# Kernel optimization log

Hardware: AMD Instinct MI355X
Metric: run time of the kernel (lower is better)

## Reference

```python
import jax, jax.numpy as jnp
import numpy as np

N_EMB = 1024
EMB_DIM = 256
BETA = 0.25


def setup_inputs() -> dict:
    key = jax.random.key(0)
    k1, k2 = jax.random.split(key)
    z = jax.random.normal(k1, (32, EMB_DIM, 32, 32), dtype=jnp.float32)
    init = 1.0 / N_EMB
    emb = jax.random.uniform(k2, (N_EMB, EMB_DIM), dtype=jnp.float32,
                             minval=-init, maxval=init)
    return {"z": z, "emb": emb}


def reference(z, emb):
    # z: [B, C, H, W] -> [B, H, W, C]
    zc = jnp.transpose(z, (0, 2, 3, 1))
    z_flat = zc.reshape(-1, EMB_DIM)  # [N, D]

    # squared L2 distances: ||z||^2 + ||e||^2 - 2 z.e^T  -> [N, K]
    distances = (jnp.sum(z_flat ** 2, axis=1, keepdims=True)
                 + jnp.sum(emb ** 2, axis=1)
                 - 2.0 * (z_flat @ emb.T))
    nearest_idx = jnp.argmin(distances, axis=1)           # [N]
    nearest = jax.nn.one_hot(nearest_idx, N_EMB, dtype=jnp.float32)  # [N, K]

    # direct gather == one-hot matmul, same math
    zq = emb[nearest_idx].reshape(zc.shape)               # [B, H, W, C]

    loss = (jnp.mean((jax.lax.stop_gradient(zq) - zc) ** 2)
            + BETA * jnp.mean((zq - jax.lax.stop_gradient(zc)) ** 2))

    # straight-through estimator
    zq_st = zc + jax.lax.stop_gradient(zq - zc)

    e_mean = jnp.mean(nearest, axis=0)                    # [K]
    perplexity = jnp.exp(-jnp.sum(e_mean * jnp.log(e_mean + 1e-10)))

    zq_out = jnp.transpose(zq_st, (0, 3, 1, 2))           # back to NCHW
    return zq_out, loss, perplexity, nearest, nearest_idx[:, None]
```

## Files before the change

### kernel.cpp

```cpp
#include <hip/hip_runtime.h>

#define N_EMB  1024
#define EMB_D  256
#define HW     1024

#define OUT_ZQ      0
#define OUT_LOSS    8388608
#define OUT_PERP    8388609
#define OUT_NEAREST 8388610
#define OUT_IDX     41943042

#define WS_HIST   0
#define WS_ESQ    4096
#define WS_LOSSP  8192
#define WS_EH     16384
#define WS_TOTAL  540672

typedef unsigned long long ull;
typedef _Float16 half8 __attribute__((ext_vector_type(8)));
typedef float f32x4 __attribute__((ext_vector_type(4)));
typedef ull ull2 __attribute__((ext_vector_type(2)));

#define L_A     0
#define L_B     32768
#define L_ESQ   49152
#define L_ZSQ   53248
#define L_WIN   53504
#define L_RED   53760
#define L_TOT   55808

__device__ __forceinline__ void gload16(const void* g, void* l) {
    __builtin_amdgcn_global_load_lds(
        (const __attribute__((address_space(1))) unsigned int*)g,
        (__attribute__((address_space(3))) unsigned int*)l, 16, 0, 0);
}

__device__ __forceinline__ float pairwise8_combine(const float r[8]) {
    return __fadd_rn(__fadd_rn(__fadd_rn(r[0], r[1]), __fadd_rn(r[2], r[3])),
                     __fadd_rn(__fadd_rn(r[4], r[5]), __fadd_rn(r[6], r[7])));
}

__global__ void prep(const float* __restrict__ emb, _Float16* __restrict__ eh,
                     float* __restrict__ esq, int* __restrict__ hist) {
    int bid = blockIdx.x;
    if (bid < 1024) {
        int c = bid, k = threadIdx.x;
        eh[c * EMB_D + k] = (_Float16)emb[c * EMB_D + k];
        return;
    }
    int c = (bid - 1024) * 256 + threadIdx.x;
    const float* p = emb + (size_t)c * EMB_D;
    float tot[2];
    #pragma unroll
    for (int h = 0; h < 2; ++h) {
        float r[8];
        #pragma unroll
        for (int i = 0; i < 8; ++i) {
            float x = p[h * 128 + i];
            r[i] = __fmul_rn(x, x);
        }
        for (int k = 8; k < 128; k += 8) {
            #pragma unroll
            for (int i = 0; i < 8; ++i) {
                float x = p[h * 128 + k + i];
                r[i] = __fadd_rn(r[i], __fmul_rn(x, x));
            }
        }
        tot[h] = pairwise8_combine(r);
    }
    esq[c] = __fadd_rn(tot[0], tot[1]);
    hist[c] = 0;
}

__global__ __launch_bounds__(256) void fused_vq(
        const float* __restrict__ z, const float* __restrict__ emb,
        const _Float16* __restrict__ eh, const float* __restrict__ esq,
        float* __restrict__ out, int* __restrict__ hist,
        double* __restrict__ lossp) {
    __shared__ __align__(16) char lds[L_TOT];
    int t = threadIdx.x, bid = blockIdx.x;
    int b = bid >> 4, hw0 = (bid & 15) << 6;
    int lane = t & 63, wave = t >> 6;
    int wm = wave >> 1, wn = wave & 1;
    int l15 = lane & 15, lq = lane >> 4;

    if (t >= 128) {
        int i = t - 128;
        #pragma unroll
        for (int q = 0; q < 2; ++q) {
            f32x4 v = *(const f32x4*)(esq + (q * 128 + i) * 4);
            *(f32x4*)(lds + L_ESQ + (q * 128 + i) * 16) = v;
        }
    } else {
        int nl = t & 63, h = (t >> 6) & 1;
        const float* zp = z + ((size_t)b << 18) + hw0 + nl;
        int kb = h << 7;
        int abase = L_A + nl * 512;
        int sw = (nl & 7) << 4;
        float r[8];
        {   half8 hv;
            #pragma unroll
            for (int e = 0; e < 8; ++e) {
                float x = zp[(size_t)(kb + e) << 10];
                hv[e] = (_Float16)x;
                r[e] = __fmul_rn(x, x);
            }
            *(half8*)(lds + abase + (((kb << 1)) ^ sw)) = hv;
        }
        for (int c8 = 1; c8 < 16; ++c8) {
            half8 hv;
            #pragma unroll
            for (int e = 0; e < 8; ++e) {
                float x = zp[(size_t)(kb + c8 * 8 + e) << 10];
                hv[e] = (_Float16)x;
                r[e] = __fadd_rn(r[e], __fmul_rn(x, x));
            }
            *(half8*)(lds + abase + (((kb << 1) + c8 * 16) ^ sw)) = hv;
        }
        *(float*)(lds + L_RED + (h * 64 + nl) * 4) = pairwise8_combine(r);
    }
    __syncthreads();
    if (t < 64) {
        float t0 = *(float*)(lds + L_RED + t * 4);
        float t1 = *(float*)(lds + L_RED + 256 + t * 4);
        *(float*)(lds + L_ZSQ + t * 4) = __fadd_rn(t0, t1);
    }
    __syncthreads();

    int aoffs[2][2], boffs[4][2];
    #pragma unroll
    for (int i = 0; i < 2; ++i) {
        int r = wm * 32 + i * 16 + l15;
        #pragma unroll
        for (int kc = 0; kc < 2; ++kc)
            aoffs[i][kc] = L_A + r * 512 + ((kc * 64 + lq * 16) ^ ((r & 7) << 4));
    }
    #pragma unroll
    for (int j = 0; j < 4; ++j) {
        int c = wn * 64 + j * 16 + l15;
        #pragma unroll
        for (int kc = 0; kc < 2; ++kc)
            boffs[j][kc] = L_B + c * 128 + ((kc * 64 + lq * 16) ^ ((c & 7) << 4));
    }
    int bsrc[4], bdst[4];
    #pragma unroll
    for (int is = 0; is < 4; ++is) {
        int o = is * 4096 + t * 16;
        int col = o >> 7;
        int K = (o & 127) ^ ((col & 7) << 4);
        bsrc[is] = col * 256 + (K >> 1);
        bdst[is] = L_B + o;
    }
    float zs[8];
    #pragma unroll
    for (int s = 0; s < 8; ++s) {
        int row = wm * 32 + (s >> 2) * 16 + lq * 4 + (s & 3);
        zs[s] = *(const float*)(lds + L_ZSQ + row * 4);
    }
    ull k1[8], k2[8];
    #pragma unroll
    for (int s = 0; s < 8; ++s) { k1[s] = ~0ULL; k2[s] = ~0ULL; }

    float* nbase = out + OUT_NEAREST + (((size_t)bid * 64) << 10);
    const f32x4 zzero = {0.f, 0.f, 0.f, 0.f};

    for (int cbt = 0; cbt < 8; ++cbt) {
        f32x4 acc[2][4];
        #pragma unroll
        for (int i = 0; i < 2; ++i)
            #pragma unroll
            for (int j = 0; j < 4; ++j) acc[i][j] = (f32x4){0.f, 0.f, 0.f, 0.f};

        for (int kt = 0; kt < 4; ++kt) {
            const int r = cbt * 4 + kt;
            __syncthreads();
            #pragma unroll
            for (int is = 0; is < 4; ++is)
                gload16(eh + cbt * 32768 + kt * 64 + bsrc[is], lds + bdst[is]);
            {
                float* zp0 = nbase + (((size_t)(2 * r + (t >> 7))) << 10) + (t & 127) * 8;
                *(f32x4*)zp0 = zzero;
                *(f32x4*)(zp0 + 4) = zzero;
            }
            __syncthreads();

            half8 a[2][2], bb[4][2];
            #pragma unroll
            for (int i = 0; i < 2; ++i) {
                a[i][0] = *(const half8*)(lds + aoffs[i][0] + kt * 128);
                a[i][1] = *(const half8*)(lds + aoffs[i][1] + kt * 128);
            }
            #pragma unroll
            for (int j = 0; j < 4; ++j) {
                bb[j][0] = *(const half8*)(lds + boffs[j][0]);
                bb[j][1] = *(const half8*)(lds + boffs[j][1]);
            }
            #pragma unroll
            for (int i = 0; i < 2; ++i)
                #pragma unroll
                for (int j = 0; j < 4; ++j) {
                    acc[i][j] = __builtin_amdgcn_mfma_f32_16x16x32_f16(a[i][0], bb[j][0], acc[i][j], 0, 0, 0);
                    acc[i][j] = __builtin_amdgcn_mfma_f32_16x16x32_f16(a[i][1], bb[j][1], acc[i][j], 0, 0, 0);
                }
        }
        float es[4];
        #pragma unroll
        for (int j = 0; j < 4; ++j)
            es[j] = *(const float*)(lds + L_ESQ + ((cbt << 7) + wn * 64 + j * 16 + l15) * 4);
        #pragma unroll
        for (int i = 0; i < 2; ++i)
            #pragma unroll
            for (int r = 0; r < 4; ++r) {
                const int s = i * 4 + r;
                float zsv = zs[s];
                #pragma unroll
                for (int j = 0; j < 4; ++j) {
                    float d = __fsub_rn(__fadd_rn(zsv, es[j]), __fmul_rn(2.0f, acc[i][j][r]));
                    int cg = (cbt << 7) + wn * 64 + j * 16 + l15;
                    ull key = ((ull)__float_as_uint(d) << 32) | (unsigned)cg;
                    if (key < k1[s]) { k2[s] = k1[s]; k1[s] = key; }
                    else if (key < k2[s]) { k2[s] = key; }
                }
            }
    }

    __syncthreads();
    #pragma unroll
    for (int s = 0; s < 8; ++s) {
        int row = wm * 32 + (s >> 2) * 16 + lq * 4 + (s & 3);
        *(ull2*)(lds + L_A + row * 512 + ((wn << 4) + l15) * 16) = (ull2){k1[s], k2[s]};
    }
    __syncthreads();

    for (int rr = 0; rr < 16; ++rr) {
        int row = wave * 16 + rr;
        ull k = *(const ull*)(lds + L_A + row * 512 + lane * 8);
        ull kmin = k;
        #pragma unroll
        for (int m = 1; m < 64; m <<= 1) {
            ull o = __shfl_xor(kmin, m, 64);
            kmin = o < kmin ? o : kmin;
        }
        float dmin = __uint_as_float((unsigned)(kmin >> 32));
        float dme  = __uint_as_float((unsigned)(k >> 32));
        bool cand = dme <= __fadd_rn(dmin, 2e-4f);
        ull bal = __ballot(cand);
        int winner;
        if (__popcll(bal) == 1) {
            winner = (int)(unsigned)(kmin & 0xFFFFFFFFu);
        } else {
            const float* zp2 = z + ((size_t)b << 18) + hw0 + row;
            float zr[4];
            #pragma unroll
            for (int e = 0; e < 4; ++e) zr[e] = zp2[(size_t)(lane + 64 * e) << 10];
            float zsr = *(const float*)(lds + L_ZSQ + row * 4);
            ull bestk = ~0ULL;
            while (bal) {
                int src = __ffsll(bal) - 1;
                bal &= bal - 1;
                ull ck = __shfl(k, src, 64);
                int c = (int)(unsigned)(ck & 0xFFFFFFFFu);
                const float* ep = emb + (size_t)c * EMB_D;
                float p = __fmul_rn(zr[3], ep[lane + 192]);
                p = __builtin_fmaf(zr[2], ep[lane + 128], p);
                p = __builtin_fmaf(zr[1], ep[lane + 64], p);
                p = __builtin_fmaf(zr[0], ep[lane], p);
                #pragma unroll
                for (int m = 1; m < 64; m <<= 1)
                    p = __fadd_rn(p, __shfl_xor(p, m, 64));
                float ec = *(const float*)(lds + L_ESQ + c * 4);
                float d = __fsub_rn(__fadd_rn(zsr, ec), __fmul_rn(2.0f, p));
                ull kk = ((ull)__float_as_uint(d) << 32) | (unsigned)c;
                bestk = kk < bestk ? kk : bestk;
            }
            winner = (int)(unsigned)(bestk & 0xFFFFFFFFu);
        }
        size_t n = (size_t)bid * 64 + row;
        if (lane == 0) {
            out[OUT_NEAREST + (n << 10) + winner] = 1.0f;
            out[OUT_IDX + n] = (float)winner;
            atomicAdd(&hist[winner], 1);
            *(int*)(lds + L_WIN + row * 4) = winner;
        }
    }
    __syncthreads();

    {
        int q = t & 15;
        int cq = t >> 4;
        int4 w4 = *(const int4*)(lds + L_WIN + q * 16);
        const float* zb = z + ((size_t)b << 18) + hw0 + q * 4;
        float* ob = out + OUT_ZQ + ((size_t)b << 18) + hw0 + q * 4;
        double s = 0.0;
        for (int i = 0; i < 16; ++i) {
            int c = cq + (i << 4);
            f32x4 zc = *(const f32x4*)(zb + ((size_t)c << 10));
            f32x4 ev = { emb[(size_t)w4.x * EMB_D + c], emb[(size_t)w4.y * EMB_D + c],
                         emb[(size_t)w4.z * EMB_D + c], emb[(size_t)w4.w * EMB_D + c] };
            f32x4 df = { __fsub_rn(ev[0], zc[0]), __fsub_rn(ev[1], zc[1]),
                         __fsub_rn(ev[2], zc[2]), __fsub_rn(ev[3], zc[3]) };
            f32x4 st = { __fadd_rn(zc[0], df[0]), __fadd_rn(zc[1], df[1]),
                         __fadd_rn(zc[2], df[2]), __fadd_rn(zc[3], df[3]) };
            *(f32x4*)(ob + ((size_t)c << 10)) = st;
            s += (double)__fmul_rn(df[0], df[0]) + (double)__fmul_rn(df[1], df[1])
               + (double)__fmul_rn(df[2], df[2]) + (double)__fmul_rn(df[3], df[3]);
        }
        *(double*)(lds + L_RED + t * 8) = s;
        __syncthreads();
        for (int st = 128; st > 0; st >>= 1) {
            if (t < st) {
                double o = *(double*)(lds + L_RED + (t + st) * 8);
                *(double*)(lds + L_RED + t * 8) += o;
            }
            __syncthreads();
        }
        if (t == 0) lossp[bid] = *(double*)(lds + L_RED);
    }
}

__global__ void finalize_scalars(const double* __restrict__ lossp,
                                 const int* __restrict__ hist,
                                 float* __restrict__ out_loss,
                                 float* __restrict__ out_perp) {
    __shared__ double sd[1024];
    int t = threadIdx.x;

    sd[t] = (t < 512) ? lossp[t] : 0.0;
    __syncthreads();
    for (int st = 512; st > 0; st >>= 1) {
        if (t < st) sd[t] += sd[t + st];
        __syncthreads();
    }
    if (t == 0) {
        double loss = 1.25 * (sd[0] / 8388608.0);
        *out_loss = (float)loss;
    }
    __syncthreads();

    float p = (float)hist[t] * (1.0f / 32768.0f);
    float term = __fmul_rn(p, logf(__fadd_rn(p, 1e-10f)));
    sd[t] = (double)term;
    __syncthreads();
    for (int st = 512; st > 0; st >>= 1) {
        if (t < st) sd[t] += sd[t + st];
        __syncthreads();
    }
    if (t == 0) *out_perp = expf(-(float)sd[0]);
}

extern "C" void kernel_launch(void* const* d_in, const int* in_sizes, int n_in,
                              void* d_out, int out_size, void* d_ws, size_t ws_size,
                              hipStream_t stream) {
    const float* z   = (const float*)d_in[0];
    const float* emb = (const float*)d_in[1];
    float* out = (float*)d_out;
    char*  ws  = (char*)d_ws;

    int*      hist  = (int*)(ws + WS_HIST);
    float*    esq   = (float*)(ws + WS_ESQ);
    double*   lossp = (double*)(ws + WS_LOSSP);
    _Float16* eh    = (_Float16*)(ws + WS_EH);

    prep<<<1028, 256, 0, stream>>>(emb, eh, esq, hist);
    fused_vq<<<512, 256, 0, stream>>>(z, emb, eh, esq, out, hist, lossp);
    finalize_scalars<<<1, 1024, 0, stream>>>(lossp, hist,
                                             out + OUT_LOSS, out + OUT_PERP);
}
```

Before: 88.82 us.

## Load codebook B fragments directly from global and write one-hot rows in one pass

```diff
diff --git a/kernel.cpp b/kernel.cpp
--- a/kernel.cpp
+++ b/kernel.cpp
@@ -22,18 +22,11 @@
 typedef ull ull2 __attribute__((ext_vector_type(2)));
 
 #define L_A     0
-#define L_B     32768
-#define L_ESQ   49152
-#define L_ZSQ   53248
-#define L_WIN   53504
-#define L_RED   53760
-#define L_TOT   55808
-
-__device__ __forceinline__ void gload16(const void* g, void* l) {
-    __builtin_amdgcn_global_load_lds(
-        (const __attribute__((address_space(1))) unsigned int*)g,
-        (__attribute__((address_space(3))) unsigned int*)l, 16, 0, 0);
-}
+#define L_ESQ   32768
+#define L_ZSQ   36864
+#define L_WIN   37120
+#define L_RED   37376
+#define L_TOT   39424
 
 __device__ __forceinline__ float pairwise8_combine(const float r[8]) {
     return __fadd_rn(__fadd_rn(__fadd_rn(r[0], r[1]), __fadd_rn(r[2], r[3])),
@@ -127,30 +120,15 @@
     }
     __syncthreads();
 
-    int aoffs[2][2], boffs[4][2];
+    int abase2[2], aswz[2];
     #pragma unroll
     for (int i = 0; i < 2; ++i) {
         int r = wm * 32 + i * 16 + l15;
-        #pragma unroll
-        for (int kc = 0; kc < 2; ++kc)
-            aoffs[i][kc] = L_A + r * 512 + ((kc * 64 + lq * 16) ^ ((r & 7) << 4));
-    }
-    #pragma unroll
-    for (int j = 0; j < 4; ++j) {
-        int c = wn * 64 + j * 16 + l15;
-        #pragma unroll
-        for (int kc = 0; kc < 2; ++kc)
-            boffs[j][kc] = L_B + c * 128 + ((kc * 64 + lq * 16) ^ ((c & 7) << 4));
-    }
-    int bsrc[4], bdst[4];
-    #pragma unroll
-    for (int is = 0; is < 4; ++is) {
-        int o = is * 4096 + t * 16;
-        int col = o >> 7;
-        int K = (o & 127) ^ ((col & 7) << 4);
-        bsrc[is] = col * 256 + (K >> 1);
-        bdst[is] = L_B + o;
-    }
+        abase2[i] = L_A + r * 512;
+        aswz[i] = (r & 7) << 4;
+    }
+    const _Float16* ehB = eh + ((size_t)(wn * 64 + l15)) * 256 + lq * 8;
+
     float zs[8];
     #pragma unroll
     for (int s = 0; s < 8; ++s) {
@@ -161,9 +139,6 @@
     #pragma unroll
     for (int s = 0; s < 8; ++s) { k1[s] = ~0ULL; k2[s] = ~0ULL; }
 
-    float* nbase = out + OUT_NEAREST + (((size_t)bid * 64) << 10);
-    const f32x4 zzero = {0.f, 0.f, 0.f, 0.f};
-
     for (int cbt = 0; cbt < 8; ++cbt) {
         f32x4 acc[2][4];
         #pragma unroll
@@ -171,38 +146,25 @@
             #pragma unroll
             for (int j = 0; j < 4; ++j) acc[i][j] = (f32x4){0.f, 0.f, 0.f, 0.f};
 
-        for (int kt = 0; kt < 4; ++kt) {
-            const int r = cbt * 4 + kt;
-            __syncthreads();
-            #pragma unroll
-            for (int is = 0; is < 4; ++is)
-                gload16(eh + cbt * 32768 + kt * 64 + bsrc[is], lds + bdst[is]);
-            {
-                float* zp0 = nbase + (((size_t)(2 * r + (t >> 7))) << 10) + (t & 127) * 8;
-                *(f32x4*)zp0 = zzero;
-                *(f32x4*)(zp0 + 4) = zzero;
-            }
-            __syncthreads();
-
-            half8 a[2][2], bb[4][2];
-            #pragma unroll
-            for (int i = 0; i < 2; ++i) {
-                a[i][0] = *(const half8*)(lds + aoffs[i][0] + kt * 128);
-                a[i][1] = *(const half8*)(lds + aoffs[i][1] + kt * 128);
-            }
-            #pragma unroll
-            for (int j = 0; j < 4; ++j) {
-                bb[j][0] = *(const half8*)(lds + boffs[j][0]);
-                bb[j][1] = *(const half8*)(lds + boffs[j][1]);
-            }
-            #pragma unroll
-            for (int i = 0; i < 2; ++i)
-                #pragma unroll
-                for (int j = 0; j < 4; ++j) {
-                    acc[i][j] = __builtin_amdgcn_mfma_f32_16x16x32_f16(a[i][0], bb[j][0], acc[i][j], 0, 0, 0);
-                    acc[i][j] = __builtin_amdgcn_mfma_f32_16x16x32_f16(a[i][1], bb[j][1], acc[i][j], 0, 0, 0);
-                }
-        }
+        const _Float16* ehT = ehB + (size_t)cbt * 32768;
+        #pragma unroll
+        for (int kk = 0; kk < 8; ++kk) {
+            half8 a0 = *(const half8*)(lds + abase2[0] + ((kk * 64 + lq * 16) ^ aswz[0]));
+            half8 a1 = *(const half8*)(lds + abase2[1] + ((kk * 64 + lq * 16) ^ aswz[1]));
+            half8 b0 = *(const half8*)(ehT + 0 * 4096 + kk * 32);
+            half8 b1 = *(const half8*)(ehT + 1 * 4096 + kk * 32);
+            half8 b2 = *(const half8*)(ehT + 2 * 4096 + kk * 32);
+            half8 b3 = *(const half8*)(ehT + 3 * 4096 + kk * 32);
+            acc[0][0] = __builtin_amdgcn_mfma_f32_16x16x32_f16(a0, b0, acc[0][0], 0, 0, 0);
+            acc[0][1] = __builtin_amdgcn_mfma_f32_16x16x32_f16(a0, b1, acc[0][1], 0, 0, 0);
+            acc[0][2] = __builtin_amdgcn_mfma_f32_16x16x32_f16(a0, b2, acc[0][2], 0, 0, 0);
+            acc[0][3] = __builtin_amdgcn_mfma_f32_16x16x32_f16(a0, b3, acc[0][3], 0, 0, 0);
+            acc[1][0] = __builtin_amdgcn_mfma_f32_16x16x32_f16(a1, b0, acc[1][0], 0, 0, 0);
+            acc[1][1] = __builtin_amdgcn_mfma_f32_16x16x32_f16(a1, b1, acc[1][1], 0, 0, 0);
+            acc[1][2] = __builtin_amdgcn_mfma_f32_16x16x32_f16(a1, b2, acc[1][2], 0, 0, 0);
+            acc[1][3] = __builtin_amdgcn_mfma_f32_16x16x32_f16(a1, b3, acc[1][3], 0, 0, 0);
+        }
+
         float es[4];
         #pragma unroll
         for (int j = 0; j < 4; ++j)
@@ -270,14 +232,21 @@
                     p = __fadd_rn(p, __shfl_xor(p, m, 64));
                 float ec = *(const float*)(lds + L_ESQ + c * 4);
                 float d = __fsub_rn(__fadd_rn(zsr, ec), __fmul_rn(2.0f, p));
-                ull kk = ((ull)__float_as_uint(d) << 32) | (unsigned)c;
-                bestk = kk < bestk ? kk : bestk;
+                ull kk2 = ((ull)__float_as_uint(d) << 32) | (unsigned)c;
+                bestk = kk2 < bestk ? kk2 : bestk;
             }
             winner = (int)(unsigned)(bestk & 0xFFFFFFFFu);
         }
         size_t n = (size_t)bid * 64 + row;
+        float* np = out + OUT_NEAREST + (n << 10);
+        #pragma unroll
+        for (int q = 0; q < 4; ++q) {
+            int c4 = q * 256 + lane * 4;
+            f32x4 v = { winner == c4     ? 1.f : 0.f, winner == c4 + 1 ? 1.f : 0.f,
+                        winner == c4 + 2 ? 1.f : 0.f, winner == c4 + 3 ? 1.f : 0.f };
+            *(f32x4*)(np + c4) = v;
+        }
         if (lane == 0) {
-            out[OUT_NEAREST + (n << 10) + winner] = 1.0f;
             out[OUT_IDX + n] = (float)winner;
             atomicAdd(&hist[winner], 1);
             *(int*)(lds + L_WIN + row * 4) = winner;
```

New measurement: 120.7 us. 1.36x slower.

## Halve rows per block, double grid, write one-hot rows densely after argmin

Applied to the files above, without the earlier changes.

```diff
diff --git a/kernel.cpp b/kernel.cpp
--- a/kernel.cpp
+++ b/kernel.cpp
@@ -22,12 +22,12 @@
 typedef ull ull2 __attribute__((ext_vector_type(2)));
 
 #define L_A     0
-#define L_B     32768
-#define L_ESQ   49152
-#define L_ZSQ   53248
-#define L_WIN   53504
-#define L_RED   53760
-#define L_TOT   55808
+#define L_B     16384
+#define L_ESQ   32768
+#define L_ZSQ   36864
+#define L_WIN   36992
+#define L_RED   37120
+#define L_TOT   39168
 
 __device__ __forceinline__ void gload16(const void* g, void* l) {
     __builtin_amdgcn_global_load_lds(
@@ -72,27 +72,20 @@
     hist[c] = 0;
 }
 
-__global__ __launch_bounds__(256) void fused_vq(
+__global__ __launch_bounds__(256, 4) void fused_vq(
         const float* __restrict__ z, const float* __restrict__ emb,
         const _Float16* __restrict__ eh, const float* __restrict__ esq,
         float* __restrict__ out, int* __restrict__ hist,
         double* __restrict__ lossp) {
     __shared__ __align__(16) char lds[L_TOT];
     int t = threadIdx.x, bid = blockIdx.x;
-    int b = bid >> 4, hw0 = (bid & 15) << 6;
+    int b = bid >> 5, hw0 = (bid & 31) << 5;
     int lane = t & 63, wave = t >> 6;
     int wm = wave >> 1, wn = wave & 1;
     int l15 = lane & 15, lq = lane >> 4;
 
-    if (t >= 128) {
-        int i = t - 128;
-        #pragma unroll
-        for (int q = 0; q < 2; ++q) {
-            f32x4 v = *(const f32x4*)(esq + (q * 128 + i) * 4);
-            *(f32x4*)(lds + L_ESQ + (q * 128 + i) * 16) = v;
-        }
-    } else {
-        int nl = t & 63, h = (t >> 6) & 1;
+    if (t < 64) {
+        int nl = t & 31, h = (t >> 5) & 1;
         const float* zp = z + ((size_t)b << 18) + hw0 + nl;
         int kb = h << 7;
         int abase = L_A + nl * 512;
@@ -117,23 +110,29 @@
             }
             *(half8*)(lds + abase + (((kb << 1) + c8 * 16) ^ sw)) = hv;
         }
-        *(float*)(lds + L_RED + (h * 64 + nl) * 4) = pairwise8_combine(r);
-    }
-    __syncthreads();
-    if (t < 64) {
+        *(float*)(lds + L_RED + (h * 32 + nl) * 4) = pairwise8_combine(r);
+    } else if (t >= 128) {
+        int i = t - 128;
+        #pragma unroll
+        for (int q = 0; q < 2; ++q) {
+            f32x4 v = *(const f32x4*)(esq + (q * 128 + i) * 4);
+            *(f32x4*)(lds + L_ESQ + (q * 128 + i) * 16) = v;
+        }
+    }
+    __syncthreads();
+    if (t < 32) {
         float t0 = *(float*)(lds + L_RED + t * 4);
-        float t1 = *(float*)(lds + L_RED + 256 + t * 4);
+        float t1 = *(float*)(lds + L_RED + 128 + t * 4);
         *(float*)(lds + L_ZSQ + t * 4) = __fadd_rn(t0, t1);
     }
     __syncthreads();
 
-    int aoffs[2][2], boffs[4][2];
-    #pragma unroll
-    for (int i = 0; i < 2; ++i) {
-        int r = wm * 32 + i * 16 + l15;
+    int aoffs[2], boffs[4][2];
+    {
+        int r = wm * 16 + l15;
         #pragma unroll
         for (int kc = 0; kc < 2; ++kc)
-            aoffs[i][kc] = L_A + r * 512 + ((kc * 64 + lq * 16) ^ ((r & 7) << 4));
+            aoffs[kc] = L_A + r * 512 + ((kc * 64 + lq * 16) ^ ((r & 7) << 4));
     }
     #pragma unroll
     for (int j = 0; j < 4; ++j) {
@@ -151,89 +150,68 @@
         bsrc[is] = col * 256 + (K >> 1);
         bdst[is] = L_B + o;
     }
-    float zs[8];
-    #pragma unroll
-    for (int s = 0; s < 8; ++s) {
-        int row = wm * 32 + (s >> 2) * 16 + lq * 4 + (s & 3);
-        zs[s] = *(const float*)(lds + L_ZSQ + row * 4);
-    }
-    ull k1[8], k2[8];
-    #pragma unroll
-    for (int s = 0; s < 8; ++s) { k1[s] = ~0ULL; k2[s] = ~0ULL; }
-
-    float* nbase = out + OUT_NEAREST + (((size_t)bid * 64) << 10);
-    const f32x4 zzero = {0.f, 0.f, 0.f, 0.f};
+    float zs[4];
+    #pragma unroll
+    for (int s = 0; s < 4; ++s)
+        zs[s] = *(const float*)(lds + L_ZSQ + (wm * 16 + lq * 4 + s) * 4);
+    ull k1[4], k2[4];
+    #pragma unroll
+    for (int s = 0; s < 4; ++s) { k1[s] = ~0ULL; k2[s] = ~0ULL; }
 
     for (int cbt = 0; cbt < 8; ++cbt) {
-        f32x4 acc[2][4];
-        #pragma unroll
-        for (int i = 0; i < 2; ++i)
-            #pragma unroll
-            for (int j = 0; j < 4; ++j) acc[i][j] = (f32x4){0.f, 0.f, 0.f, 0.f};
+        f32x4 acc[4];
+        #pragma unroll
+        for (int j = 0; j < 4; ++j) acc[j] = (f32x4){0.f, 0.f, 0.f, 0.f};
 
         for (int kt = 0; kt < 4; ++kt) {
-            const int r = cbt * 4 + kt;
             __syncthreads();
             #pragma unroll
             for (int is = 0; is < 4; ++is)
                 gload16(eh + cbt * 32768 + kt * 64 + bsrc[is], lds + bdst[is]);
-            {
-                float* zp0 = nbase + (((size_t)(2 * r + (t >> 7))) << 10) + (t & 127) * 8;
-                *(f32x4*)zp0 = zzero;
-                *(f32x4*)(zp0 + 4) = zzero;
-            }
             __syncthreads();
 
-            half8 a[2][2], bb[4][2];
-            #pragma unroll
-            for (int i = 0; i < 2; ++i) {
-                a[i][0] = *(const half8*)(lds + aoffs[i][0] + kt * 128);
-                a[i][1] = *(const half8*)(lds + aoffs[i][1] + kt * 128);
-            }
+            half8 a0 = *(const half8*)(lds + aoffs[0] + kt * 128);
+            half8 a1 = *(const half8*)(lds + aoffs[1] + kt * 128);
+            half8 bb[4][2];
             #pragma unroll
             for (int j = 0; j < 4; ++j) {
                 bb[j][0] = *(const half8*)(lds + boffs[j][0]);
                 bb[j][1] = *(const half8*)(lds + boffs[j][1]);
             }
             #pragma unroll
-            for (int i = 0; i < 2; ++i)
-                #pragma unroll
-                for (int j = 0; j < 4; ++j) {
-                    acc[i][j] = __builtin_amdgcn_mfma_f32_16x16x32_f16(a[i][0], bb[j][0], acc[i][j], 0, 0, 0);
-                    acc[i][j] = __builtin_amdgcn_mfma_f32_16x16x32_f16(a[i][1], bb[j][1], acc[i][j], 0, 0, 0);
-                }
+            for (int j = 0; j < 4; ++j) {
+                acc[j] = __builtin_amdgcn_mfma_f32_16x16x32_f16(a0, bb[j][0], acc[j], 0, 0, 0);
+                acc[j] = __builtin_amdgcn_mfma_f32_16x16x32_f16(a1, bb[j][1], acc[j], 0, 0, 0);
+            }
         }
         float es[4];
         #pragma unroll
         for (int j = 0; j < 4; ++j)
             es[j] = *(const float*)(lds + L_ESQ + ((cbt << 7) + wn * 64 + j * 16 + l15) * 4);
         #pragma unroll
-        for (int i = 0; i < 2; ++i)
-            #pragma unroll
-            for (int r = 0; r < 4; ++r) {
-                const int s = i * 4 + r;
-                float zsv = zs[s];
-                #pragma unroll
-                for (int j = 0; j < 4; ++j) {
-                    float d = __fsub_rn(__fadd_rn(zsv, es[j]), __fmul_rn(2.0f, acc[i][j][r]));
-                    int cg = (cbt << 7) + wn * 64 + j * 16 + l15;
-                    ull key = ((ull)__float_as_uint(d) << 32) | (unsigned)cg;
-                    if (key < k1[s]) { k2[s] = k1[s]; k1[s] = key; }
-                    else if (key < k2[s]) { k2[s] = key; }
-                }
-            }
-    }
-
-    __syncthreads();
-    #pragma unroll
-    for (int s = 0; s < 8; ++s) {
-        int row = wm * 32 + (s >> 2) * 16 + lq * 4 + (s & 3);
+        for (int s = 0; s < 4; ++s) {
+            float zsv = zs[s];
+            #pragma unroll
+            for (int j = 0; j < 4; ++j) {
+                float d = __fsub_rn(__fadd_rn(zsv, es[j]), __fmul_rn(2.0f, acc[j][s]));
+                int cg = (cbt << 7) + wn * 64 + j * 16 + l15;
+                ull key = ((ull)__float_as_uint(d) << 32) | (unsigned)cg;
+                if (key < k1[s]) { k2[s] = k1[s]; k1[s] = key; }
+                else if (key < k2[s]) { k2[s] = key; }
+            }
+        }
+    }
+
+    __syncthreads();
+    #pragma unroll
+    for (int s = 0; s < 4; ++s) {
+        int row = wm * 16 + lq * 4 + s;
         *(ull2*)(lds + L_A + row * 512 + ((wn << 4) + l15) * 16) = (ull2){k1[s], k2[s]};
     }
     __syncthreads();
 
-    for (int rr = 0; rr < 16; ++rr) {
-        int row = wave * 16 + rr;
+    for (int rr = 0; rr < 8; ++rr) {
+        int row = wave * 8 + rr;
         ull k = *(const ull*)(lds + L_A + row * 512 + lane * 8);
         ull kmin = k;
         #pragma unroll
@@ -270,14 +248,21 @@
                     p = __fadd_rn(p, __shfl_xor(p, m, 64));
                 float ec = *(const float*)(lds + L_ESQ + c * 4);
                 float d = __fsub_rn(__fadd_rn(zsr, ec), __fmul_rn(2.0f, p));
-                ull kk = ((ull)__float_as_uint(d) << 32) | (unsigned)c;
-                bestk = kk < bestk ? kk : bestk;
+                ull kk2 = ((ull)__float_as_uint(d) << 32) | (unsigned)c;
+                bestk = kk2 < bestk ? kk2 : bestk;
             }
             winner = (int)(unsigned)(bestk & 0xFFFFFFFFu);
         }
-        size_t n = (size_t)bid * 64 + row;
+        size_t n = (size_t)bid * 32 + row;
+        float* np = out + OUT_NEAREST + (n << 10);
+        #pragma unroll
+        for (int q = 0; q < 4; ++q) {
+            int c4 = q * 256 + lane * 4;
+            f32x4 v = { winner == c4     ? 1.f : 0.f, winner == c4 + 1 ? 1.f : 0.f,
+                        winner == c4 + 2 ? 1.f : 0.f, winner == c4 + 3 ? 1.f : 0.f };
+            *(f32x4*)(np + c4) = v;
+        }
         if (lane == 0) {
-            out[OUT_NEAREST + (n << 10) + winner] = 1.0f;
             out[OUT_IDX + n] = (float)winner;
             atomicAdd(&hist[winner], 1);
             *(int*)(lds + L_WIN + row * 4) = winner;
@@ -286,14 +271,15 @@
     __syncthreads();
 
     {
-        int q = t & 15;
-        int cq = t >> 4;
+        int q = t & 7;
+        int cq = t >> 3;
         int4 w4 = *(const int4*)(lds + L_WIN + q * 16);
         const float* zb = z + ((size_t)b << 18) + hw0 + q * 4;
         float* ob = out + OUT_ZQ + ((size_t)b << 18) + hw0 + q * 4;
         double s = 0.0;
-        for (int i = 0; i < 16; ++i) {
-            int c = cq + (i << 4);
+        #pragma unroll
+        for (int i = 0; i < 8; ++i) {
+            int c = cq + (i << 5);
             f32x4 zc = *(const f32x4*)(zb + ((size_t)c << 10));
             f32x4 ev = { emb[(size_t)w4.x * EMB_D + c], emb[(size_t)w4.y * EMB_D + c],
                          emb[(size_t)w4.z * EMB_D + c], emb[(size_t)w4.w * EMB_D + c] };
@@ -325,7 +311,7 @@
     __shared__ double sd[1024];
     int t = threadIdx.x;
 
-    sd[t] = (t < 512) ? lossp[t] : 0.0;
+    sd[t] = lossp[t];
     __syncthreads();
     for (int st = 512; st > 0; st >>= 1) {
         if (t < st) sd[t] += sd[t + st];
@@ -362,7 +348,7 @@
     _Float16* eh    = (_Float16*)(ws + WS_EH);
 
     prep<<<1028, 256, 0, stream>>>(emb, eh, esq, hist);
-    fused_vq<<<512, 256, 0, stream>>>(z, emb, eh, esq, out, hist, lossp);
+    fused_vq<<<1024, 256, 0, stream>>>(z, emb, eh, esq, out, hist, lossp);
     finalize_scalars<<<1, 1024, 0, stream>>>(lossp, hist,
                                              out + OUT_LOSS, out + OUT_PERP);
 }
```

New measurement: 82.08 us. 7.6% less time.
